# Performance work log

Hardware: AMD Instinct MI355X
Metric: run time of the kernel (lower is better)

Reference implementation:

```python
import jax, jax.numpy as jnp
import numpy as np

B, N, D, H, E, C = 32, 1024, 256, 256, 256, 256
K = 128          # top-k retained clusters = C // top_ratio
TEMP = 0.1
EPS = 1e-15


def _l2norm(x, eps=1e-12):
    n = jnp.linalg.norm(x, axis=-1, keepdims=True)
    return x / jnp.maximum(n, eps)


def _dense_sage(x, adj, Wr, br, Wo):
    # PyG DenseSAGEConv: mean-aggregate neighbors, lin_rel + lin_root, l2-normalize
    deg = jnp.clip(jnp.sum(adj, axis=-1, keepdims=True), 1.0, None)
    agg = jnp.matmul(adj, x) / deg                      # [B,N,D]
    out = agg @ Wr + br + x @ Wo                         # [B,N,H]
    return _l2norm(out)


def _sage_block(x, adj, Wr, br, Wo, Wl, bl):
    h = jax.nn.relu(_dense_sage(x, adj, Wr, br, Wo))
    return h @ Wl + bl


def setup_inputs() -> dict:
    key = jax.random.key(0)
    ks = jax.random.split(key, 12)
    sc = 0.05
    return {
        "x": jax.random.normal(ks[0], (B, N, D), jnp.float32),
        "adj": jax.random.uniform(ks[1], (B, N, N), jnp.float32),
        # pool branch (out = C clusters)
        "Wr_p": jax.random.normal(ks[2], (D, H), jnp.float32) * sc,
        "br_p": jnp.zeros((H,), jnp.float32),
        "Wo_p": jax.random.normal(ks[3], (D, H), jnp.float32) * sc,
        "Wl_p": jax.random.normal(ks[4], (H, C), jnp.float32) * sc,
        "bl_p": jnp.zeros((C,), jnp.float32),
        # embed branch (out = E features)
        "Wr_e": jax.random.normal(ks[5], (D, H), jnp.float32) * sc,
        "br_e": jnp.zeros((H,), jnp.float32),
        "Wo_e": jax.random.normal(ks[6], (D, H), jnp.float32) * sc,
        "Wl_e": jax.random.normal(ks[7], (H, E), jnp.float32) * sc,
        "bl_e": jnp.zeros((E,), jnp.float32),
    }


def reference(x, adj, Wr_p, br_p, Wo_p, Wl_p, bl_p, Wr_e, br_e, Wo_e, Wl_e, bl_e):
    s_logits = _sage_block(x, adj, Wr_p, br_p, Wo_p, Wl_p, bl_p)   # [B,N,C]
    node_x = _sage_block(x, adj, Wr_e, br_e, Wo_e, Wl_e, bl_e)     # [B,N,E]

    s = jax.nn.softmax(s_logits, axis=-1)

    # soft top-k cluster retain: sigmoid gate around the k-th largest column mass
    scores = jnp.sum(s, axis=1)                                    # [B,C]
    thresh = jax.lax.top_k(scores, K)[0][:, -1]                    # [B]
    gate = jax.nn.sigmoid((scores - thresh[:, None]) / TEMP)       # [B,C]
    s = s * gate[:, None, :]

    # pooled features / adjacency
    xp = jnp.einsum('bnc,bnd->bcd', s, node_x)                     # [B,C,E]
    sTa = jnp.einsum('bnc,bnm->bcm', s, adj)                       # [B,C,N]
    adj_p = jnp.einsum('bcm,bmk->bck', sTa, s)                     # [B,C,C]

    # link prediction loss: ||A - S S^T||_F / numel(A)
    ssT = jnp.einsum('bnc,bmc->bnm', s, s)
    link = jnp.linalg.norm(adj - ssT) / adj.size

    # entropy loss over assignments
    ent = jnp.mean(jnp.sum(-s * jnp.log(s + EPS), axis=-1))

    # cluster (orthogonality) loss: ||S^T S / ||S^T S||_F - I/sqrt(C)||_F
    sts = jnp.einsum('bnc,bnk->bck', s, s)                         # [B,C,C]
    sts_n = sts / jnp.maximum(
        jnp.linalg.norm(sts, axis=(-2, -1), keepdims=True), 1e-12)
    eye = jnp.eye(C, dtype=s.dtype) / jnp.sqrt(jnp.asarray(C, s.dtype))
    clu = jnp.mean(jnp.linalg.norm(sts_n - eye, axis=(-2, -1)))

    # adjacency reconstruction loss: ||A - S A_pool S^T||_F / numel(A)
    recon_adj = jnp.einsum('bnc,bck,bmk->bnm', s, adj_p, s)
    recon = jnp.linalg.norm(adj - recon_adj) / adj.size

    return (xp, adj_p, s, link, ent, clu, recon, node_x)
```

## Files before the change

kernel.cpp:

```cpp
#include <hip/hip_runtime.h>
#include <hip/hip_bf16.h>
#include <math.h>


typedef short bf16x8 __attribute__((ext_vector_type(8)));
typedef float f32x4 __attribute__((ext_vector_type(4)));
typedef unsigned short u16x8 __attribute__((ext_vector_type(8)));

__device__ inline void gl_lds16(const void* g, void* l) {
    __builtin_amdgcn_global_load_lds(
        (const __attribute__((address_space(1))) void*)g,
        (__attribute__((address_space(3))) void*)l, 16, 0, 0);
}

__device__ inline unsigned short f2b(float f) {
    union { __hip_bfloat16 h; unsigned short u; } cv;
    cv.h = __float2bfloat16(f);
    return cv.u;
}
__device__ inline float b2f(unsigned short u) {
    union { unsigned short u; __hip_bfloat16 h; } cv;
    cv.u = u;
    return __bfloat162float(cv.h);
}

__global__ __launch_bounds__(256) void adjconv_kernel(
    const float* __restrict__ adj, unsigned short* __restrict__ adj_bf,
    float* __restrict__ deginv, float* __restrict__ asq_part) {
    __shared__ float sq_red[4];
    const int tid = threadIdx.x;
    const int wave = tid >> 6, lane = tid & 63;
    const long long row = (long long)blockIdx.x * 4 + wave;
    const float* ip = adj + row * 1024;
    unsigned short* op = adj_bf + row * 1024;
    float sum = 0.f, sq = 0.f;
#pragma unroll
    for (int i = 0; i < 2; ++i) {
        const float4 v0 = *(const float4*)(ip + i * 512 + lane * 8);
        const float4 v1 = *(const float4*)(ip + i * 512 + lane * 8 + 4);
        u16x8 h;
        h[0] = f2b(v0.x); h[1] = f2b(v0.y); h[2] = f2b(v0.z); h[3] = f2b(v0.w);
        h[4] = f2b(v1.x); h[5] = f2b(v1.y); h[6] = f2b(v1.z); h[7] = f2b(v1.w);
        *(u16x8*)(op + i * 512 + lane * 8) = h;
        sum += (v0.x + v0.y + v0.z + v0.w) + (v1.x + v1.y + v1.z + v1.w);
        sq = fmaf(v0.x, v0.x, sq); sq = fmaf(v0.y, v0.y, sq);
        sq = fmaf(v0.z, v0.z, sq); sq = fmaf(v0.w, v0.w, sq);
        sq = fmaf(v1.x, v1.x, sq); sq = fmaf(v1.y, v1.y, sq);
        sq = fmaf(v1.z, v1.z, sq); sq = fmaf(v1.w, v1.w, sq);
    }
#pragma unroll
    for (int off = 32; off > 0; off >>= 1) {
        sum += __shfl_xor(sum, off);
        sq  += __shfl_xor(sq, off);
    }
    if (lane == 0) {
        deginv[row] = 1.0f / fmaxf(sum, 1.0f);
        sq_red[wave] = sq;
    }
    __syncthreads();
    if (tid == 0)
        asq_part[blockIdx.x] = sq_red[0] + sq_red[1] + sq_red[2] + sq_red[3];
}

__global__ __launch_bounds__(256) void convt_kernel(
    const float* __restrict__ in, long long sIn, int ldin,
    unsigned short* __restrict__ outN, long long sN,
    unsigned short* __restrict__ outT, long long sT, int ldT) {
    __shared__ float tile[64][65];
    const int tid = threadIdx.x;
    const long long bz = blockIdx.z;
    const int rowBase = blockIdx.y * 64, colBase = blockIdx.x * 64;
    const float* ip = in + bz * sIn;
#pragma unroll
    for (int i = 0; i < 4; ++i) {
        int r = (tid >> 4) * 4 + i;
        const float4 v = *(const float4*)(ip + (long long)(rowBase + r) * ldin + colBase + (tid & 15) * 4);
        tile[r][(tid & 15) * 4 + 0] = v.x;
        tile[r][(tid & 15) * 4 + 1] = v.y;
        tile[r][(tid & 15) * 4 + 2] = v.z;
        tile[r][(tid & 15) * 4 + 3] = v.w;
        if (outN) {
            ushort4 h;
            h.x = f2b(v.x); h.y = f2b(v.y); h.z = f2b(v.z); h.w = f2b(v.w);
            *(ushort4*)(outN + bz * sN + (long long)(rowBase + r) * ldin + colBase + (tid & 15) * 4) = h;
        }
    }
    __syncthreads();
    if (outT) {
#pragma unroll
        for (int i = 0; i < 4; ++i) {
            int oc = (tid >> 4) * 4 + i;
            ushort4 h;
            h.x = f2b(tile[(tid & 15) * 4 + 0][oc]);
            h.y = f2b(tile[(tid & 15) * 4 + 1][oc]);
            h.z = f2b(tile[(tid & 15) * 4 + 2][oc]);
            h.w = f2b(tile[(tid & 15) * 4 + 3][oc]);
            *(ushort4*)(outT + bz * sT + (long long)(colBase + oc) * ldT + rowBase + (tid & 15) * 4) = h;
        }
    }
}

struct WPtrs { const float* in[6]; unsigned short* out[6]; };
__global__ __launch_bounds__(256) void wconv_kernel(WPtrs wp) {
    __shared__ float tile[64][65];
    const int tid = threadIdx.x;
    const float* in = wp.in[blockIdx.z];
    unsigned short* out = wp.out[blockIdx.z];
    const int rowBase = blockIdx.y * 64, colBase = blockIdx.x * 64;
#pragma unroll
    for (int i = 0; i < 4; ++i) {
        int r = (tid >> 4) * 4 + i;
        const float4 v = *(const float4*)(in + (long long)(rowBase + r) * 256 + colBase + (tid & 15) * 4);
        tile[r][(tid & 15) * 4 + 0] = v.x;
        tile[r][(tid & 15) * 4 + 1] = v.y;
        tile[r][(tid & 15) * 4 + 2] = v.z;
        tile[r][(tid & 15) * 4 + 3] = v.w;
    }
    __syncthreads();
#pragma unroll
    for (int i = 0; i < 4; ++i) {
        int oc = (tid >> 4) * 4 + i;
        ushort4 h;
        h.x = f2b(tile[(tid & 15) * 4 + 0][oc]);
        h.y = f2b(tile[(tid & 15) * 4 + 1][oc]);
        h.z = f2b(tile[(tid & 15) * 4 + 2][oc]);
        h.w = f2b(tile[(tid & 15) * 4 + 3][oc]);
        *(ushort4*)(out + (long long)(colBase + oc) * 256 + rowBase + (tid & 15) * 4) = h;
    }
}

struct GemmP {
    const unsigned short* A1; long long sA1; int lda1; int K1;
    const unsigned short* B1; long long sB1; int ldb1;
    const unsigned short* A2; long long sA2; int lda2; int K2;
    const unsigned short* B2; long long sB2; int ldb2;
    float* outF; long long sF;
    unsigned short* outH; long long sH;
    unsigned short* outT; long long sT; int ldt;
    int ldc;
    const float* bias;
    const float* rowscale; long long sRS;
    const unsigned short* dotN; long long sDot;
    float* dot_part;
    float* sq_part;
};

__global__ __launch_bounds__(256) void gemm_mfma(GemmP p) {
    __shared__ char smem[32768];
    __shared__ float dred[256];
    const int tid = threadIdx.x;
    const int wave = tid >> 6, lane = tid & 63;
    const int quad = lane >> 4, l15 = lane & 15;
    const int wm = (wave & 1) * 64, wn = (wave >> 1) * 64;
    const long long bz = blockIdx.z;
    const int rowBase = blockIdx.y * 128, colBase = blockIdx.x * 128;
    const int srow = tid >> 2;
    const int skg = (((tid & 3) ^ ((srow >> 1) & 3)) * 8);
    const int rsw = (l15 >> 1) & 3;

    const int n1 = p.K1 >> 5;
    const int n2 = p.A2 ? (p.K2 >> 5) : 0;
    const int nTot = n1 + n2;

    const unsigned short* A1p = p.A1 + bz * p.sA1;
    const unsigned short* B1p = p.B1 + bz * p.sB1;
    const unsigned short* A2p = p.A2 ? p.A2 + bz * p.sA2 : nullptr;
    const unsigned short* B2p = p.B2 ? p.B2 + bz * p.sB2 : nullptr;

    auto stage = [&](int t, int buf) {
        const unsigned short *Ao, *Bo; int lda, ldb, ko;
        if (t < n1) { Ao = A1p; Bo = B1p; lda = p.lda1; ldb = p.ldb1; ko = t * 32; }
        else        { Ao = A2p; Bo = B2p; lda = p.lda2; ldb = p.ldb2; ko = (t - n1) * 32; }
        char* la = smem + buf * 16384 + wave * 1024;
        char* lb = smem + buf * 16384 + 8192 + wave * 1024;
        gl_lds16(Ao + (long long)(rowBase + srow) * lda + ko + skg, la);
        gl_lds16(Ao + (long long)(rowBase + 64 + srow) * lda + ko + skg, la + 4096);
        gl_lds16(Bo + (long long)(colBase + srow) * ldb + ko + skg, lb);
        gl_lds16(Bo + (long long)(colBase + 64 + srow) * ldb + ko + skg, lb + 4096);
    };

    f32x4 acc[4][4] = {{{0.f}}};
    stage(0, 0);
    __syncthreads();
    int cur = 0;
    for (int t = 0; t < nTot; ++t) {
        if (t + 1 < nTot) stage(t + 1, cur ^ 1);
        const short* Ab = (const short*)(smem + cur * 16384);
        const short* Bb = (const short*)(smem + cur * 16384 + 8192);
        bf16x8 af[4], bf[4];
#pragma unroll
        for (int i = 0; i < 4; ++i)
            af[i] = *(const bf16x8*)(Ab + (wm + i * 16 + l15) * 32 + (quad ^ rsw) * 8);
#pragma unroll
        for (int j = 0; j < 4; ++j)
            bf[j] = *(const bf16x8*)(Bb + (wn + j * 16 + l15) * 32 + (quad ^ rsw) * 8);
#pragma unroll
        for (int i = 0; i < 4; ++i)
#pragma unroll
            for (int j = 0; j < 4; ++j)
                acc[i][j] = __builtin_amdgcn_mfma_f32_16x16x32_bf16(af[i], bf[j], acc[i][j], 0, 0, 0);
        __syncthreads();
        cur ^= 1;
    }

    float* oF = p.outF ? p.outF + bz * p.sF : nullptr;
    unsigned short* oH = p.outH ? p.outH + bz * p.sH : nullptr;
    const unsigned short* dN = p.dotN ? p.dotN + bz * p.sDot : nullptr;
    unsigned short* tt = (unsigned short*)smem;
    float bcol[4];
#pragma unroll
    for (int j = 0; j < 4; ++j)
        bcol[j] = p.bias ? p.bias[colBase + wn + j * 16 + l15] : 0.0f;
    const float* rs = p.rowscale ? p.rowscale + bz * p.sRS : nullptr;
    float dacc = 0.f;
#pragma unroll
    for (int i = 0; i < 4; ++i) {
        ushort4 tp[4];
#pragma unroll
        for (int r = 0; r < 4; ++r) {
            int row = rowBase + wm + i * 16 + quad * 4 + r;
            float sc = rs ? rs[row] : 1.0f;
            long long ro = (long long)row * p.ldc;
#pragma unroll
            for (int j = 0; j < 4; ++j) {
                int col = colBase + wn + j * 16 + l15;
                float v = (acc[i][j][r] + bcol[j]) * sc;
                if (oF) oF[ro + col] = v;
                if (oH) oH[ro + col] = f2b(v);
                if (dN) dacc = fmaf(v, b2f(dN[ro + col]), dacc);
                if (p.sq_part) dacc = fmaf(v, v, dacc);
                ((unsigned short*)&tp[j])[r] = f2b(v);
            }
        }
        if (p.outT) {
            int lr = wm + i * 16 + quad * 4;
#pragma unroll
            for (int j = 0; j < 4; ++j) {
                int lc = wn + j * 16 + l15;
                *(ushort4*)&tt[lc * 128 + (lr ^ ((lc & 15) << 3))] = tp[j];
            }
        }
    }
    if (p.outT) {
        __syncthreads();
#pragma unroll
        for (int u = 0; u < 8; ++u) {
            int idx = u * 256 + tid;
            int c = idx >> 4;
            int r0 = (idx & 15) * 8;
            u16x8 val = *(const u16x8*)&tt[c * 128 + (r0 ^ ((c & 15) << 3))];
            int gr = rowBase + r0;
            long long tb = bz + (gr >> 10);
            *(u16x8*)(p.outT + tb * p.sT + (long long)(colBase + c) * p.ldt + (gr & 1023)) = val;
        }
    }
    if (p.dot_part || p.sq_part) {
        dred[tid] = dacc;
        __syncthreads();
        for (int k = 128; k > 0; k >>= 1) {
            if (tid < k) dred[tid] += dred[tid + k];
            __syncthreads();
        }
        if (tid == 0) {
            float* dst = p.dot_part ? p.dot_part : p.sq_part;
            dst[((long long)bz * gridDim.y + blockIdx.y) * gridDim.x + blockIdx.x] = dred[0];
        }
    }
}

struct SageP {
    const unsigned short* A1; const unsigned short* B1;
    const unsigned short* A2; const unsigned short* B2;
    const float* bias;
    unsigned short* out;
};

__global__ __launch_bounds__(512) void sage_mfma(SageP p) {
    __shared__ short As[2][4096];
    __shared__ short Bs[2][8192];
    __shared__ float rsum[4][128];
    const int tid = threadIdx.x;
    const int wave = tid >> 6, lane = tid & 63;
    const int quad = lane >> 4, l15 = lane & 15;
    const int wm = (wave & 1) * 64, wn = (wave >> 1) * 64;
    const int rowBase = blockIdx.x * 128;
    const int srow = tid >> 2;
    const int skg = (((tid & 3) ^ ((srow >> 1) & 3)) * 8);
    const int rsw = (l15 >> 1) & 3;

    auto stage = [&](int t, int buf) {
        const unsigned short* Ao = (t < 8) ? p.A1 : p.A2;
        const unsigned short* Bo = (t < 8) ? p.B1 : p.B2;
        int ko = (t & 7) * 32;
        char* la = (char*)As[buf] + wave * 1024;
        char* lb = (char*)Bs[buf] + wave * 1024;
        gl_lds16(Ao + (long long)(rowBase + srow) * 256 + ko + skg, la);
        gl_lds16(Bo + (long long)srow * 256 + ko + skg, lb);
        gl_lds16(Bo + (long long)(128 + srow) * 256 + ko + skg, lb + 8192);
    };

    f32x4 acc[4][4] = {{{0.f}}};
    stage(0, 0);
    __syncthreads();
    int cur = 0;
    for (int t = 0; t < 16; ++t) {
        if (t + 1 < 16) stage(t + 1, cur ^ 1);
        const short* Ab = As[cur];
        const short* Bb = Bs[cur];
        bf16x8 af[4], bf[4];
#pragma unroll
        for (int i = 0; i < 4; ++i)
            af[i] = *(const bf16x8*)(Ab + (wm + i * 16 + l15) * 32 + (quad ^ rsw) * 8);
#pragma unroll
        for (int j = 0; j < 4; ++j)
            bf[j] = *(const bf16x8*)(Bb + (wn + j * 16 + l15) * 32 + (quad ^ rsw) * 8);
#pragma unroll
        for (int i = 0; i < 4; ++i)
#pragma unroll
            for (int j = 0; j < 4; ++j)
                acc[i][j] = __builtin_amdgcn_mfma_f32_16x16x32_bf16(af[i], bf[j], acc[i][j], 0, 0, 0);
        __syncthreads();
        cur ^= 1;
    }

    float bcol[4];
#pragma unroll
    for (int j = 0; j < 4; ++j)
        bcol[j] = p.bias[wn + j * 16 + l15];

#pragma unroll
    for (int i = 0; i < 4; ++i)
#pragma unroll
        for (int r = 0; r < 4; ++r) {
            float ss = 0.f;
#pragma unroll
            for (int j = 0; j < 4; ++j) {
                float v = acc[i][j][r] + bcol[j];
                ss = fmaf(v, v, ss);
            }
#pragma unroll
            for (int off = 1; off < 16; off <<= 1) ss += __shfl_xor(ss, off);
            if (l15 == 0) rsum[wave >> 1][wm + i * 16 + quad * 4 + r] = ss;
        }
    __syncthreads();
#pragma unroll
    for (int i = 0; i < 4; ++i)
#pragma unroll
        for (int r = 0; r < 4; ++r) {
            int lrow = wm + i * 16 + quad * 4 + r;
            float tot = rsum[0][lrow] + rsum[1][lrow] + rsum[2][lrow] + rsum[3][lrow];
            float rn = 1.0f / fmaxf(sqrtf(tot), 1e-12f);
            long long ro = (long long)(rowBase + lrow) * 256;
#pragma unroll
            for (int j = 0; j < 4; ++j) {
                float v = (acc[i][j][r] + bcol[j]) * rn;
                p.out[ro + wn + j * 16 + l15] = f2b(fmaxf(v, 0.0f));
            }
        }
}

__global__ __launch_bounds__(256) void sts_clu_mfma(
    const unsigned short* __restrict__ sT, unsigned short* __restrict__ gout,
    float* __restrict__ ssq_part, float* __restrict__ tr_part) {
    __shared__ short As[2][128 * 32];
    __shared__ short Bs[2][128 * 32];
    __shared__ float red[2][256];
    const int tid = threadIdx.x;
    const int wave = tid >> 6, lane = tid & 63;
    const int quad = lane >> 4, l15 = lane & 15;
    const int wm = (wave & 1) * 64, wn = (wave >> 1) * 64;
    const long long bz = blockIdx.z;
    const unsigned short* S = sT + bz * 262144;
    const int rowBase = blockIdx.y * 128, colBase = blockIdx.x * 128;
    const int srow = tid >> 2;
    const int skg = (((tid & 3) ^ ((srow >> 1) & 3)) * 8);
    const int rsw = (l15 >> 1) & 3;

    auto stage = [&](int t, int buf) {
        int ko = t * 32;
        char* la = (char*)As + buf * 8192 + wave * 1024;
        char* lb = (char*)Bs + buf * 8192 + wave * 1024;
        gl_lds16(S + (long long)(rowBase + srow) * 1024 + ko + skg, la);
        gl_lds16(S + (long long)(rowBase + 64 + srow) * 1024 + ko + skg, la + 4096);
        gl_lds16(S + (long long)(colBase + srow) * 1024 + ko + skg, lb);
        gl_lds16(S + (long long)(colBase + 64 + srow) * 1024 + ko + skg, lb + 4096);
    };

    f32x4 acc[4][4] = {{{0.f}}};
    stage(0, 0);
    __syncthreads();
    int cur = 0;
    for (int t = 0; t < 32; ++t) {
        if (t + 1 < 32) stage(t + 1, cur ^ 1);
        const short* Ab = (const short*)((char*)As + cur * 8192);
        const short* Bb = (const short*)((char*)Bs + cur * 8192);
        bf16x8 af[4], bf[4];
#pragma unroll
        for (int i = 0; i < 4; ++i)
            af[i] = *(const bf16x8*)(Ab + (wm + i * 16 + l15) * 32 + (quad ^ rsw) * 8);
#pragma unroll
        for (int j = 0; j < 4; ++j)
            bf[j] = *(const bf16x8*)(Bb + (wn + j * 16 + l15) * 32 + (quad ^ rsw) * 8);
#pragma unroll
        for (int i = 0; i < 4; ++i)
#pragma unroll
            for (int j = 0; j < 4; ++j)
                acc[i][j] = __builtin_amdgcn_mfma_f32_16x16x32_bf16(af[i], bf[j], acc[i][j], 0, 0, 0);
        __syncthreads();
        cur ^= 1;
    }
    unsigned short* go = gout + bz * 65536;
    float ssq = 0.f, tr = 0.f;
#pragma unroll
    for (int i = 0; i < 4; ++i)
#pragma unroll
        for (int r = 0; r < 4; ++r) {
            int row = rowBase + wm + i * 16 + quad * 4 + r;
#pragma unroll
            for (int j = 0; j < 4; ++j) {
                int col = colBase + wn + j * 16 + l15;
                float v = acc[i][j][r];
                go[(long long)row * 256 + col] = f2b(v);
                ssq = fmaf(v, v, ssq);
                if (row == col) tr += v;
            }
        }
    red[0][tid] = ssq;
    red[1][tid] = tr;
    __syncthreads();
    for (int k = 128; k > 0; k >>= 1) {
        if (tid < k) {
            red[0][tid] += red[0][tid + k];
            red[1][tid] += red[1][tid + k];
        }
        __syncthreads();
    }
    if (tid == 0) {
        int bid = (int)(blockIdx.z * 4 + blockIdx.y * 2 + blockIdx.x);
        ssq_part[bid] = red[0][0];
        tr_part[bid] = red[1][0];
    }
}

__global__ __launch_bounds__(256) void trq_mfma(
    const unsigned short* __restrict__ G, const unsigned short* __restrict__ P,
    const unsigned short* __restrict__ PT, float* __restrict__ trq_part) {
    __shared__ short sm[4][2][4096];
    __shared__ float dred[256];
    const int tid = threadIdx.x;
    const int wave = tid >> 6, lane = tid & 63;
    const int quad = lane >> 4, l15 = lane & 15;
    const int wm = (wave & 1) * 64, wn = (wave >> 1) * 64;
    const long long bz = blockIdx.z;
    const int rowBase = blockIdx.y * 128, colBase = blockIdx.x * 128;
    const int srow = tid >> 2;
    const int skg = (((tid & 3) ^ ((srow >> 1) & 3)) * 8);
    const int rsw = (l15 >> 1) & 3;
    const unsigned short* Gb = G + bz * 65536;
    const unsigned short* Pb = P + bz * 65536;
    const unsigned short* PTb = PT + bz * 65536;

    auto stage = [&](int t, int buf) {
        int ko = t * 32;
#pragma unroll
        for (int h = 0; h < 2; ++h) {
            int rr = rowBase + h * 64 + srow, cc = colBase + h * 64 + srow;
            gl_lds16(Gb + (long long)rr * 256 + ko + skg, (char*)sm[0][buf] + h * 4096 + wave * 1024);
            gl_lds16(PTb + (long long)cc * 256 + ko + skg, (char*)sm[1][buf] + h * 4096 + wave * 1024);
            gl_lds16(Pb + (long long)rr * 256 + ko + skg, (char*)sm[2][buf] + h * 4096 + wave * 1024);
            gl_lds16(Gb + (long long)cc * 256 + ko + skg, (char*)sm[3][buf] + h * 4096 + wave * 1024);
        }
    };

    f32x4 a1[4][4] = {{{0.f}}};
    f32x4 a3[4][4] = {{{0.f}}};
    stage(0, 0);
    __syncthreads();
    int cur = 0;
    for (int t = 0; t < 8; ++t) {
        if (t + 1 < 8) stage(t + 1, cur ^ 1);
        bf16x8 gA[4], pB[4], pA[4], gB[4];
#pragma unroll
        for (int i = 0; i < 4; ++i) {
            int ro = (wm + i * 16 + l15) * 32 + (quad ^ rsw) * 8;
            gA[i] = *(const bf16x8*)(sm[0][cur] + ro);
            pA[i] = *(const bf16x8*)(sm[2][cur] + ro);
        }
#pragma unroll
        for (int j = 0; j < 4; ++j) {
            int co = (wn + j * 16 + l15) * 32 + (quad ^ rsw) * 8;
            pB[j] = *(const bf16x8*)(sm[1][cur] + co);
            gB[j] = *(const bf16x8*)(sm[3][cur] + co);
        }
#pragma unroll
        for (int i = 0; i < 4; ++i)
#pragma unroll
            for (int j = 0; j < 4; ++j) {
                a1[i][j] = __builtin_amdgcn_mfma_f32_16x16x32_bf16(gA[i], pB[j], a1[i][j], 0, 0, 0);
                a3[i][j] = __builtin_amdgcn_mfma_f32_16x16x32_bf16(pA[i], gB[j], a3[i][j], 0, 0, 0);
            }
        __syncthreads();
        cur ^= 1;
    }
    float dacc = 0.f;
#pragma unroll
    for (int i = 0; i < 4; ++i)
#pragma unroll
        for (int j = 0; j < 4; ++j)
#pragma unroll
            for (int r = 0; r < 4; ++r)
                dacc = fmaf(a3[i][j][r], a1[i][j][r], dacc);
    dred[tid] = dacc;
    __syncthreads();
    for (int k = 128; k > 0; k >>= 1) {
        if (tid < k) dred[tid] += dred[tid + k];
        __syncthreads();
    }
    if (tid == 0)
        trq_part[(blockIdx.z * 2 + blockIdx.y) * 2 + blockIdx.x] = dred[0];
}

__global__ __launch_bounds__(256) void smstat_kernel(
    const float* __restrict__ s, float* __restrict__ rowmax,
    float* __restrict__ rowrden, float* __restrict__ scores) {
    __shared__ float sacc[4][256];
    const int tid = threadIdx.x;
    const int wave = tid >> 6, lane = tid & 63;
    const int b = blockIdx.x >> 5;
    const long long row0 = (long long)blockIdx.x * 32;
    float c0 = 0.f, c1 = 0.f, c2 = 0.f, c3 = 0.f;
#pragma unroll
    for (int q = 0; q < 8; ++q) {
        long long row = row0 + wave * 8 + q;
        const float4 v = *(const float4*)(s + row * 256 + lane * 4);
        float m = fmaxf(fmaxf(v.x, v.y), fmaxf(v.z, v.w));
#pragma unroll
        for (int off = 32; off > 0; off >>= 1) m = fmaxf(m, __shfl_xor(m, off));
        float e0 = expf(v.x - m), e1 = expf(v.y - m);
        float e2 = expf(v.z - m), e3 = expf(v.w - m);
        float den = e0 + e1 + e2 + e3;
#pragma unroll
        for (int off = 32; off > 0; off >>= 1) den += __shfl_xor(den, off);
        float rd = 1.0f / den;
        if (lane == 0) { rowmax[row] = m; rowrden[row] = rd; }
        c0 = fmaf(e0, rd, c0); c1 = fmaf(e1, rd, c1);
        c2 = fmaf(e2, rd, c2); c3 = fmaf(e3, rd, c3);
    }
    sacc[wave][lane * 4 + 0] = c0;
    sacc[wave][lane * 4 + 1] = c1;
    sacc[wave][lane * 4 + 2] = c2;
    sacc[wave][lane * 4 + 3] = c3;
    __syncthreads();
    float t0 = sacc[0][tid] + sacc[1][tid] + sacc[2][tid] + sacc[3][tid];
    atomicAdd(&scores[b * 256 + tid], t0);
}

__global__ __launch_bounds__(256) void topkgate_kernel(const float* __restrict__ scores,
                                                       float* __restrict__ gate) {
    __shared__ float vals[256];
    __shared__ float th;
    int b = blockIdx.x, tid = threadIdx.x;
    float v = scores[b * 256 + tid];
    vals[tid] = v;
    __syncthreads();
    int rank = 0;
    for (int j = 0; j < 256; ++j) {
        float u = vals[j];
        rank += (u > v) || (u == v && j < tid);
    }
    if (rank == 127) th = v;
    __syncthreads();
    float z = (v - th) * 10.0f;
    gate[b * 256 + tid] = 1.0f / (1.0f + expf(-z));
}

__global__ __launch_bounds__(256) void gatefin_kernel(
    float* __restrict__ s, const float* __restrict__ rowmax,
    const float* __restrict__ rowrden, const float* __restrict__ gate,
    unsigned short* __restrict__ sbf, unsigned short* __restrict__ sT,
    float* __restrict__ ent_part) {
    __shared__ float tile[64][65];
    __shared__ float red[256];
    const int tid = threadIdx.x;
    const long long bz = blockIdx.z;
    const int rowBase = blockIdx.y * 64, colBase = blockIdx.x * 64;
    const int c4 = (tid & 15) * 4;
    const float g0 = gate[bz * 256 + colBase + c4 + 0];
    const float g1 = gate[bz * 256 + colBase + c4 + 1];
    const float g2 = gate[bz * 256 + colBase + c4 + 2];
    const float g3 = gate[bz * 256 + colBase + c4 + 3];
    float ent = 0.f;
#pragma unroll
    for (int i = 0; i < 4; ++i) {
        int r = (tid >> 4) * 4 + i;
        long long grow = bz * 1024 + rowBase + r;
        float4 v = *(const float4*)(s + grow * 256 + colBase + c4);
        float m = rowmax[grow], rd = rowrden[grow];
        float p0 = expf(v.x - m) * rd * g0;
        float p1 = expf(v.y - m) * rd * g1;
        float p2 = expf(v.z - m) * rd * g2;
        float p3 = expf(v.w - m) * rd * g3;
        float4 pv; pv.x = p0; pv.y = p1; pv.z = p2; pv.w = p3;
        *(float4*)(s + grow * 256 + colBase + c4) = pv;
        ushort4 h;
        h.x = f2b(p0); h.y = f2b(p1); h.z = f2b(p2); h.w = f2b(p3);
        *(ushort4*)(sbf + grow * 256 + colBase + c4) = h;
        tile[r][c4 + 0] = p0; tile[r][c4 + 1] = p1;
        tile[r][c4 + 2] = p2; tile[r][c4 + 3] = p3;
        ent -= p0 * logf(p0 + 1e-15f) + p1 * logf(p1 + 1e-15f) +
               p2 * logf(p2 + 1e-15f) + p3 * logf(p3 + 1e-15f);
    }
    __syncthreads();
#pragma unroll
    for (int i = 0; i < 4; ++i) {
        int oc = (tid >> 4) * 4 + i;
        ushort4 h;
        h.x = f2b(tile[c4 + 0][oc]);
        h.y = f2b(tile[c4 + 1][oc]);
        h.z = f2b(tile[c4 + 2][oc]);
        h.w = f2b(tile[c4 + 3][oc]);
        *(ushort4*)(sT + bz * 262144 + (long long)(colBase + oc) * 1024 + rowBase + c4) = h;
    }
    red[tid] = ent;
    __syncthreads();
    for (int k = 128; k > 0; k >>= 1) {
        if (tid < k) red[tid] += red[tid + k];
        __syncthreads();
    }
    if (tid == 0)
        ent_part[((long long)bz * gridDim.y + blockIdx.y) * gridDim.x + blockIdx.x] = red[0];
}

__global__ __launch_bounds__(256) void finalize_kernel(const float* __restrict__ ent_part,
                                                       const float* __restrict__ asq_part,
                                                       const float* __restrict__ psq_part,
                                                       const float* __restrict__ sdot_part,
                                                       const float* __restrict__ trq_part,
                                                       const float* __restrict__ ssq_part,
                                                       const float* __restrict__ tr_part,
                                                       float* __restrict__ scal) {
    __shared__ float red[7][256];
    int tid = threadIdx.x;
    float e = 0.f, asq = 0.f, psq = 0.f, sd = 0.f, tq = 0.f, clu = 0.f, ssqa = 0.f;
    for (int i = tid; i < 2048; i += 256) e += ent_part[i];
    for (int i = tid; i < 8192; i += 256) asq += asq_part[i];
    if (tid < 128) psq = psq_part[tid];
    for (int i = tid; i < 512; i += 256) sd += sdot_part[i];
    if (tid < 128) tq = trq_part[tid];
    if (tid < 32) {
        float ssq = 0.f, tr = 0.f;
#pragma unroll
        for (int i = 0; i < 4; ++i) {
            ssq += ssq_part[tid * 4 + i];
            tr  += tr_part[tid * 4 + i];
        }
        ssqa = ssq;
        float fro = fmaxf(sqrtf(ssq), 1e-12f);
        float val = ssq / (fro * fro) - tr / (8.0f * fro) + 1.0f;
        clu = sqrtf(fmaxf(val, 0.0f));
    }
    red[0][tid] = e; red[1][tid] = asq; red[2][tid] = psq; red[3][tid] = sd;
    red[4][tid] = tq; red[5][tid] = clu; red[6][tid] = ssqa;
    __syncthreads();
    for (int k = 128; k > 0; k >>= 1) {
        if (tid < k) {
#pragma unroll
            for (int q = 0; q < 7; ++q) red[q][tid] += red[q][tid + k];
        }
        __syncthreads();
    }
    if (tid == 0) {
        const float numel = 33554432.0f;
        float linksq  = red[1][0] - 2.0f * red[3][0] + red[6][0];
        float reconsq = red[1][0] - 2.0f * red[2][0] + red[4][0];
        scal[0] = sqrtf(fmaxf(linksq, 0.0f)) / numel;
        scal[1] = red[0][0] / 32768.0f;
        scal[2] = red[5][0] / 32.0f;
        scal[3] = sqrtf(fmaxf(reconsq, 0.0f)) / numel;
    }
}

extern "C" void kernel_launch(void* const* d_in, const int* in_sizes, int n_in,
                              void* d_out, int out_size, void* d_ws, size_t ws_size,
                              hipStream_t stream) {
    const float* x    = (const float*)d_in[0];
    const float* adj  = (const float*)d_in[1];
    const float* Wr_p = (const float*)d_in[2];
    const float* br_p = (const float*)d_in[3];
    const float* Wo_p = (const float*)d_in[4];
    const float* Wl_p = (const float*)d_in[5];
    const float* bl_p = (const float*)d_in[6];
    const float* Wr_e = (const float*)d_in[7];
    const float* br_e = (const float*)d_in[8];
    const float* Wo_e = (const float*)d_in[9];
    const float* Wl_e = (const float*)d_in[10];
    const float* bl_e = (const float*)d_in[11];

    float* out    = (float*)d_out;
    float* xp     = out;
    float* adj_p  = out + 2097152;
    float* s      = out + 4194304;
    float* scal   = out + 12582912;
    float* node_x = out + 12582916;

    char* w = (char*)d_ws;
    float* degsum     = (float*)w; w += 32768 * 4;
    float* scores     = (float*)w; w += 8192 * 4;
    float* thresh     = (float*)w; w += 256 * 4;
    float* gatep      = (float*)w; w += 8192 * 4;
    float* ent_part   = (float*)w; w += 32768 * 4;
    float* asq_part   = (float*)w; w += 8192 * 4;
    float* psq_part   = (float*)w; w += 512 * 4;
    float* sdot_part  = (float*)w; w += 1024 * 4;
    float* trq_part   = (float*)w; w += 256 * 4;
    float* ssq_part   = (float*)w; w += 256 * 4;
    float* tr_part    = (float*)w; w += 256 * 4;
    unsigned short* WT   = (unsigned short*)w; w += 6LL * 65536 * 2;
    unsigned short* bufA = (unsigned short*)w; w += 33554432LL * 2;
    unsigned short* bufB = (unsigned short*)w; w += 8388608LL * 2;
    unsigned short* bufC = (unsigned short*)w; w += 8388608LL * 2;
    unsigned short* bufD = (unsigned short*)w; w += 8388608LL * 2;
    unsigned short* bufE = (unsigned short*)w; w += 8388608LL * 2;
    unsigned short* bufF = (unsigned short*)w; w += 8388608LL * 2;
    unsigned short* bufG = (unsigned short*)w; w += 8388608LL * 2;
    unsigned short* bufH = (unsigned short*)w; w += 2097152LL * 2;

    unsigned short* G_bf  = bufB;
    unsigned short* PT_bf = bufB + 2097152;
    float* rowmax  = degsum;
    float* rowrden = (float*)bufH;
    (void)thresh;

    hipMemsetAsync(scores, 0, 8192 * sizeof(float), stream);

    adjconv_kernel<<<8192, 256, 0, stream>>>(adj, bufA, degsum, asq_part);

    convt_kernel<<<dim3(4, 16, 32), 256, 0, stream>>>(
        x, 262144LL, 256, bufB, 262144LL, bufC, 262144LL, 1024);

    WPtrs wp;
    wp.in[0] = Wr_p; wp.in[1] = Wo_p; wp.in[2] = Wl_p;
    wp.in[3] = Wr_e; wp.in[4] = Wo_e; wp.in[5] = Wl_e;
    for (int i = 0; i < 6; ++i) wp.out[i] = WT + (long long)i * 65536;
    wconv_kernel<<<dim3(4, 4, 6), 256, 0, stream>>>(wp);

    GemmP g;
    g = {};
    g.A1 = bufA; g.sA1 = 1048576; g.lda1 = 1024; g.K1 = 1024;
    g.B1 = bufC; g.sB1 = 262144; g.ldb1 = 1024;
    g.outH = bufD; g.sH = 262144; g.ldc = 256;
    g.rowscale = degsum; g.sRS = 1024;
    gemm_mfma<<<dim3(2, 8, 32), 256, 0, stream>>>(g);

    SageP sp;
    sp.A1 = bufD; sp.B1 = WT + 0 * 65536;
    sp.A2 = bufB; sp.B2 = WT + 1 * 65536;
    sp.bias = br_p; sp.out = bufE;
    sage_mfma<<<256, 512, 0, stream>>>(sp);

    g = {};
    g.A1 = bufE; g.sA1 = 0; g.lda1 = 256; g.K1 = 256; g.B1 = WT + 2 * 65536; g.sB1 = 0; g.ldb1 = 256;
    g.outF = s; g.sF = 0; g.ldc = 256; g.bias = bl_p;
    gemm_mfma<<<dim3(2, 256, 1), 256, 0, stream>>>(g);

    sp.A1 = bufD; sp.B1 = WT + 3 * 65536;
    sp.A2 = bufB; sp.B2 = WT + 4 * 65536;
    sp.bias = br_e; sp.out = bufE;
    sage_mfma<<<256, 512, 0, stream>>>(sp);

    g = {};
    g.A1 = bufE; g.sA1 = 0; g.lda1 = 256; g.K1 = 256; g.B1 = WT + 5 * 65536; g.sB1 = 0; g.ldb1 = 256;
    g.outF = node_x; g.sF = 0; g.ldc = 256; g.bias = bl_e;
    g.outT = bufD; g.sT = 262144; g.ldt = 1024;
    gemm_mfma<<<dim3(2, 256, 1), 256, 0, stream>>>(g);

    smstat_kernel<<<1024, 256, 0, stream>>>(s, rowmax, rowrden, scores);
    topkgate_kernel<<<32, 256, 0, stream>>>(scores, gatep);
    gatefin_kernel<<<dim3(4, 16, 32), 256, 0, stream>>>(
        s, rowmax, rowrden, gatep, bufG, bufC, ent_part);

    g = {};
    g.A1 = bufC; g.sA1 = 262144; g.lda1 = 1024; g.K1 = 1024;
    g.B1 = bufD; g.sB1 = 262144; g.ldb1 = 1024;
    g.outF = xp; g.sF = 65536; g.ldc = 256;
    gemm_mfma<<<dim3(2, 2, 32), 256, 0, stream>>>(g);

    g = {};
    g.A1 = bufA; g.sA1 = 1048576; g.lda1 = 1024; g.K1 = 1024;
    g.B1 = bufC; g.sB1 = 262144; g.ldb1 = 1024;
    g.ldc = 256;
    g.outT = bufF; g.sT = 262144; g.ldt = 1024;
    g.dotN = bufG; g.sDot = 262144; g.dot_part = sdot_part;
    gemm_mfma<<<dim3(2, 8, 32), 256, 0, stream>>>(g);

    sts_clu_mfma<<<dim3(2, 2, 32), 256, 0, stream>>>(bufC, G_bf, ssq_part, tr_part);

    g = {};
    g.A1 = bufC; g.sA1 = 262144; g.lda1 = 1024; g.K1 = 1024;
    g.B1 = bufF; g.sB1 = 262144; g.ldb1 = 1024;
    g.outF = adj_p; g.sF = 65536; g.ldc = 256;
    g.outH = bufH; g.sH = 65536;
    g.outT = PT_bf; g.sT = 65536; g.ldt = 256;
    g.sq_part = psq_part;
    gemm_mfma<<<dim3(2, 2, 32), 256, 0, stream>>>(g);

    trq_mfma<<<dim3(2, 2, 32), 256, 0, stream>>>(G_bf, bufH, PT_bf, trq_part);

    finalize_kernel<<<1, 256, 0, stream>>>(ent_part, asq_part, psq_part, sdot_part,
                                           trq_part, ssq_part, tr_part, scal);
}
```

Before: 580.0 us.

## Fuse adjacency conversion into aggregation GEMM, merge xp and S^T S GEMMs

Adjacency bf16 conversion, degree and squared-norm reduction now run inside a new aggregation MFMA kernel. It reads fp32 adj straight from global memory and feeds the converted tile into LDS, which removes the separate conversion pass and the later re-read of bf16 adj. The xp and S^T S GEMMs now share one kernel that loads the S^T tile once for both products. The pooling logits are also stored as bf16 instead of fp32, which cuts memory traffic but reduces softmax input precision.

```diff
diff --git a/kernel.cpp b/kernel.cpp
--- a/kernel.cpp
+++ b/kernel.cpp
@@ -22,44 +22,6 @@
     union { unsigned short u; __hip_bfloat16 h; } cv;
     cv.u = u;
     return __bfloat162float(cv.h);
-}
-
-__global__ __launch_bounds__(256) void adjconv_kernel(
-    const float* __restrict__ adj, unsigned short* __restrict__ adj_bf,
-    float* __restrict__ deginv, float* __restrict__ asq_part) {
-    __shared__ float sq_red[4];
-    const int tid = threadIdx.x;
-    const int wave = tid >> 6, lane = tid & 63;
-    const long long row = (long long)blockIdx.x * 4 + wave;
-    const float* ip = adj + row * 1024;
-    unsigned short* op = adj_bf + row * 1024;
-    float sum = 0.f, sq = 0.f;
-#pragma unroll
-    for (int i = 0; i < 2; ++i) {
-        const float4 v0 = *(const float4*)(ip + i * 512 + lane * 8);
-        const float4 v1 = *(const float4*)(ip + i * 512 + lane * 8 + 4);
-        u16x8 h;
-        h[0] = f2b(v0.x); h[1] = f2b(v0.y); h[2] = f2b(v0.z); h[3] = f2b(v0.w);
-        h[4] = f2b(v1.x); h[5] = f2b(v1.y); h[6] = f2b(v1.z); h[7] = f2b(v1.w);
-        *(u16x8*)(op + i * 512 + lane * 8) = h;
-        sum += (v0.x + v0.y + v0.z + v0.w) + (v1.x + v1.y + v1.z + v1.w);
-        sq = fmaf(v0.x, v0.x, sq); sq = fmaf(v0.y, v0.y, sq);
-        sq = fmaf(v0.z, v0.z, sq); sq = fmaf(v0.w, v0.w, sq);
-        sq = fmaf(v1.x, v1.x, sq); sq = fmaf(v1.y, v1.y, sq);
-        sq = fmaf(v1.z, v1.z, sq); sq = fmaf(v1.w, v1.w, sq);
-    }
-#pragma unroll
-    for (int off = 32; off > 0; off >>= 1) {
-        sum += __shfl_xor(sum, off);
-        sq  += __shfl_xor(sq, off);
-    }
-    if (lane == 0) {
-        deginv[row] = 1.0f / fmaxf(sum, 1.0f);
-        sq_red[wave] = sq;
-    }
-    __syncthreads();
-    if (tid == 0)
-        asq_part[blockIdx.x] = sq_red[0] + sq_red[1] + sq_red[2] + sq_red[3];
 }
 
 __global__ __launch_bounds__(256) void convt_kernel(
@@ -129,6 +91,110 @@
     }
 }
 
+struct AggP {
+    const float* adj;
+    const unsigned short* xT;
+    unsigned short* adj_bf;
+    unsigned short* agg;
+    float* asq_part;
+};
+
+__global__ __launch_bounds__(512) void aggdeg_mfma(AggP p) {
+    __shared__ short As[2][128 * 32];
+    __shared__ short Bs[2][256 * 32];
+    __shared__ float deginv_lds[128];
+    __shared__ float sred[512];
+    const int tid = threadIdx.x;
+    const int wave = tid >> 6, lane = tid & 63;
+    const int quad = lane >> 4, l15 = lane & 15;
+    const int wm = (wave & 1) * 64, wn = (wave >> 1) * 64;
+    const int rowBase = blockIdx.x * 128;
+    const long long bz = blockIdx.y;
+    const int srow = tid >> 2, kq = tid & 3;
+    const int sw = (srow >> 1) & 3;
+    const int skg = ((kq ^ sw) * 8);
+    const int rsw = (l15 >> 1) & 3;
+
+    const float* adjp = p.adj + bz * 1048576 + (long long)(rowBase + srow) * 1024 + kq * 8;
+    unsigned short* abf = p.adj_bf + bz * 1048576 + (long long)(rowBase + srow) * 1024 + kq * 8;
+    const unsigned short* xTp = p.xT + bz * 262144;
+
+    float4 ra, rb;
+    float degacc = 0.f, sqacc = 0.f;
+
+    auto loadA = [&](int t) {
+        ra = *(const float4*)(adjp + t * 32);
+        rb = *(const float4*)(adjp + t * 32 + 4);
+    };
+    auto procA = [&](int t, int buf) {
+        u16x8 h;
+        h[0] = f2b(ra.x); h[1] = f2b(ra.y); h[2] = f2b(ra.z); h[3] = f2b(ra.w);
+        h[4] = f2b(rb.x); h[5] = f2b(rb.y); h[6] = f2b(rb.z); h[7] = f2b(rb.w);
+        *(u16x8*)(abf + t * 32) = h;
+        degacc += (ra.x + ra.y + ra.z + ra.w) + (rb.x + rb.y + rb.z + rb.w);
+        sqacc = fmaf(ra.x, ra.x, sqacc); sqacc = fmaf(ra.y, ra.y, sqacc);
+        sqacc = fmaf(ra.z, ra.z, sqacc); sqacc = fmaf(ra.w, ra.w, sqacc);
+        sqacc = fmaf(rb.x, rb.x, sqacc); sqacc = fmaf(rb.y, rb.y, sqacc);
+        sqacc = fmaf(rb.z, rb.z, sqacc); sqacc = fmaf(rb.w, rb.w, sqacc);
+        *(u16x8*)((unsigned short*)As[buf] + srow * 32 + ((kq ^ sw) * 8)) = h;
+    };
+    auto stageB = [&](int t, int buf) {
+        char* lb = (char*)Bs[buf] + wave * 1024;
+        gl_lds16(xTp + (long long)srow * 1024 + t * 32 + skg, lb);
+        gl_lds16(xTp + (long long)(128 + srow) * 1024 + t * 32 + skg, lb + 8192);
+    };
+
+    f32x4 acc[4][4] = {{{0.f}}};
+    loadA(0);
+    stageB(0, 0);
+    procA(0, 0);
+    __syncthreads();
+    int cur = 0;
+    for (int t = 0; t < 32; ++t) {
+        const bool more = (t + 1 < 32);
+        if (more) { loadA(t + 1); stageB(t + 1, cur ^ 1); }
+        bf16x8 af[4], bv[4];
+#pragma unroll
+        for (int i = 0; i < 4; ++i)
+            af[i] = *(const bf16x8*)(As[cur] + (wm + i * 16 + l15) * 32 + (quad ^ rsw) * 8);
+#pragma unroll
+        for (int j = 0; j < 4; ++j)
+            bv[j] = *(const bf16x8*)(Bs[cur] + (wn + j * 16 + l15) * 32 + (quad ^ rsw) * 8);
+#pragma unroll
+        for (int i = 0; i < 4; ++i)
+#pragma unroll
+            for (int j = 0; j < 4; ++j)
+                acc[i][j] = __builtin_amdgcn_mfma_f32_16x16x32_bf16(af[i], bv[j], acc[i][j], 0, 0, 0);
+        if (more) procA(t + 1, cur ^ 1);
+        __syncthreads();
+        cur ^= 1;
+    }
+
+    degacc += __shfl_xor(degacc, 1);
+    degacc += __shfl_xor(degacc, 2);
+    if (kq == 0) deginv_lds[srow] = 1.0f / fmaxf(degacc, 1.0f);
+    sred[tid] = sqacc;
+    __syncthreads();
+    for (int k = 256; k > 0; k >>= 1) {
+        if (tid < k) sred[tid] += sred[tid + k];
+        __syncthreads();
+    }
+    if (tid == 0) p.asq_part[bz * 8 + blockIdx.x] = sred[0];
+
+    unsigned short* og = p.agg + bz * 262144;
+#pragma unroll
+    for (int i = 0; i < 4; ++i)
+#pragma unroll
+        for (int r = 0; r < 4; ++r) {
+            int lrow = wm + i * 16 + quad * 4 + r;
+            float sc = deginv_lds[lrow];
+            long long ro = (long long)(rowBase + lrow) * 256;
+#pragma unroll
+            for (int j = 0; j < 4; ++j)
+                og[ro + wn + j * 16 + l15] = f2b(acc[i][j][r] * sc);
+        }
+}
+
 struct GemmP {
     const unsigned short* A1; long long sA1; int lda1; int K1;
     const unsigned short* B1; long long sB1; int ldb1;
@@ -139,7 +205,6 @@
     unsigned short* outT; long long sT; int ldt;
     int ldc;
     const float* bias;
-    const float* rowscale; long long sRS;
     const unsigned short* dotN; long long sDot;
     float* dot_part;
     float* sq_part;
@@ -211,7 +276,6 @@
 #pragma unroll
     for (int j = 0; j < 4; ++j)
         bcol[j] = p.bias ? p.bias[colBase + wn + j * 16 + l15] : 0.0f;
-    const float* rs = p.rowscale ? p.rowscale + bz * p.sRS : nullptr;
     float dacc = 0.f;
 #pragma unroll
     for (int i = 0; i < 4; ++i) {
@@ -219,12 +283,11 @@
 #pragma unroll
         for (int r = 0; r < 4; ++r) {
             int row = rowBase + wm + i * 16 + quad * 4 + r;
-            float sc = rs ? rs[row] : 1.0f;
             long long ro = (long long)row * p.ldc;
 #pragma unroll
             for (int j = 0; j < 4; ++j) {
                 int col = colBase + wn + j * 16 + l15;
-                float v = (acc[i][j][r] + bcol[j]) * sc;
+                float v = acc[i][j][r] + bcol[j];
                 if (oF) oF[ro + col] = v;
                 if (oH) oH[ro + col] = f2b(v);
                 if (dN) dacc = fmaf(v, b2f(dN[ro + col]), dacc);
@@ -359,11 +422,11 @@
         }
 }
 
-__global__ __launch_bounds__(256) void sts_clu_mfma(
-    const unsigned short* __restrict__ sT, unsigned short* __restrict__ gout,
+__global__ __launch_bounds__(256) void xpg_mfma(
+    const unsigned short* __restrict__ sT, const unsigned short* __restrict__ nxT,
+    float* __restrict__ xp, unsigned short* __restrict__ gout,
     float* __restrict__ ssq_part, float* __restrict__ tr_part) {
-    __shared__ short As[2][128 * 32];
-    __shared__ short Bs[2][128 * 32];
+    __shared__ char smem[49152];
     __shared__ float red[2][256];
     const int tid = threadIdx.x;
     const int wave = tid >> 6, lane = tid & 63;
@@ -371,6 +434,7 @@
     const int wm = (wave & 1) * 64, wn = (wave >> 1) * 64;
     const long long bz = blockIdx.z;
     const unsigned short* S = sT + bz * 262144;
+    const unsigned short* NX = nxT + bz * 262144;
     const int rowBase = blockIdx.y * 128, colBase = blockIdx.x * 128;
     const int srow = tid >> 2;
     const int skg = (((tid & 3) ^ ((srow >> 1) & 3)) * 8);
@@ -378,37 +442,49 @@
 
     auto stage = [&](int t, int buf) {
         int ko = t * 32;
-        char* la = (char*)As + buf * 8192 + wave * 1024;
-        char* lb = (char*)Bs + buf * 8192 + wave * 1024;
+        char* la = smem + buf * 8192 + wave * 1024;
+        char* l1 = smem + 16384 + buf * 8192 + wave * 1024;
+        char* l2 = smem + 32768 + buf * 8192 + wave * 1024;
         gl_lds16(S + (long long)(rowBase + srow) * 1024 + ko + skg, la);
         gl_lds16(S + (long long)(rowBase + 64 + srow) * 1024 + ko + skg, la + 4096);
-        gl_lds16(S + (long long)(colBase + srow) * 1024 + ko + skg, lb);
-        gl_lds16(S + (long long)(colBase + 64 + srow) * 1024 + ko + skg, lb + 4096);
+        gl_lds16(NX + (long long)(colBase + srow) * 1024 + ko + skg, l1);
+        gl_lds16(NX + (long long)(colBase + 64 + srow) * 1024 + ko + skg, l1 + 4096);
+        gl_lds16(S + (long long)(colBase + srow) * 1024 + ko + skg, l2);
+        gl_lds16(S + (long long)(colBase + 64 + srow) * 1024 + ko + skg, l2 + 4096);
     };
 
-    f32x4 acc[4][4] = {{{0.f}}};
+    f32x4 a1[4][4] = {{{0.f}}};
+    f32x4 a2[4][4] = {{{0.f}}};
     stage(0, 0);
     __syncthreads();
     int cur = 0;
     for (int t = 0; t < 32; ++t) {
         if (t + 1 < 32) stage(t + 1, cur ^ 1);
-        const short* Ab = (const short*)((char*)As + cur * 8192);
-        const short* Bb = (const short*)((char*)Bs + cur * 8192);
-        bf16x8 af[4], bf[4];
+        const short* Ab  = (const short*)(smem + cur * 8192);
+        const short* B1b = (const short*)(smem + 16384 + cur * 8192);
+        const short* B2b = (const short*)(smem + 32768 + cur * 8192);
+        bf16x8 af[4], b1[4], b2[4];
 #pragma unroll
         for (int i = 0; i < 4; ++i)
             af[i] = *(const bf16x8*)(Ab + (wm + i * 16 + l15) * 32 + (quad ^ rsw) * 8);
 #pragma unroll
-        for (int j = 0; j < 4; ++j)
-            bf[j] = *(const bf16x8*)(Bb + (wn + j * 16 + l15) * 32 + (quad ^ rsw) * 8);
+        for (int j = 0; j < 4; ++j) {
+            int co = (wn + j * 16 + l15) * 32 + (quad ^ rsw) * 8;
+            b1[j] = *(const bf16x8*)(B1b + co);
+            b2[j] = *(const bf16x8*)(B2b + co);
+        }
 #pragma unroll
         for (int i = 0; i < 4; ++i)
 #pragma unroll
-            for (int j = 0; j < 4; ++j)
-                acc[i][j] = __builtin_amdgcn_mfma_f32_16x16x32_bf16(af[i], bf[j], acc[i][j], 0, 0, 0);
+            for (int j = 0; j < 4; ++j) {
+                a1[i][j] = __builtin_amdgcn_mfma_f32_16x16x32_bf16(af[i], b1[j], a1[i][j], 0, 0, 0);
+                a2[i][j] = __builtin_amdgcn_mfma_f32_16x16x32_bf16(af[i], b2[j], a2[i][j], 0, 0, 0);
+            }
         __syncthreads();
         cur ^= 1;
     }
+
+    float* xo = xp + bz * 65536;
     unsigned short* go = gout + bz * 65536;
     float ssq = 0.f, tr = 0.f;
 #pragma unroll
@@ -416,11 +492,13 @@
 #pragma unroll
         for (int r = 0; r < 4; ++r) {
             int row = rowBase + wm + i * 16 + quad * 4 + r;
+            long long ro = (long long)row * 256;
 #pragma unroll
             for (int j = 0; j < 4; ++j) {
                 int col = colBase + wn + j * 16 + l15;
-                float v = acc[i][j][r];
-                go[(long long)row * 256 + col] = f2b(v);
+                xo[ro + col] = a1[i][j][r];
+                float v = a2[i][j][r];
+                go[ro + col] = f2b(v);
                 ssq = fmaf(v, v, ssq);
                 if (row == col) tr += v;
             }
@@ -521,7 +599,7 @@
 }
 
 __global__ __launch_bounds__(256) void smstat_kernel(
-    const float* __restrict__ s, float* __restrict__ rowmax,
+    const unsigned short* __restrict__ s, float* __restrict__ rowmax,
     float* __restrict__ rowrden, float* __restrict__ scores) {
     __shared__ float sacc[4][256];
     const int tid = threadIdx.x;
@@ -532,12 +610,13 @@
 #pragma unroll
     for (int q = 0; q < 8; ++q) {
         long long row = row0 + wave * 8 + q;
-        const float4 v = *(const float4*)(s + row * 256 + lane * 4);
-        float m = fmaxf(fmaxf(v.x, v.y), fmaxf(v.z, v.w));
+        const ushort4 v4 = *(const ushort4*)(s + row * 256 + lane * 4);
+        float vx = b2f(v4.x), vy = b2f(v4.y), vz = b2f(v4.z), vw = b2f(v4.w);
+        float m = fmaxf(fmaxf(vx, vy), fmaxf(vz, vw));
 #pragma unroll
         for (int off = 32; off > 0; off >>= 1) m = fmaxf(m, __shfl_xor(m, off));
-        float e0 = expf(v.x - m), e1 = expf(v.y - m);
-        float e2 = expf(v.z - m), e3 = expf(v.w - m);
+        float e0 = expf(vx - m), e1 = expf(vy - m);
+        float e2 = expf(vz - m), e3 = expf(vw - m);
         float den = e0 + e1 + e2 + e3;
 #pragma unroll
         for (int off = 32; off > 0; off >>= 1) den += __shfl_xor(den, off);
@@ -575,10 +654,10 @@
 }
 
 __global__ __launch_bounds__(256) void gatefin_kernel(
-    float* __restrict__ s, const float* __restrict__ rowmax,
-    const float* __restrict__ rowrden, const float* __restrict__ gate,
-    unsigned short* __restrict__ sbf, unsigned short* __restrict__ sT,
-    float* __restrict__ ent_part) {
+    const unsigned short* slog, float* __restrict__ s,
+    const float* __restrict__ rowmax, const float* __restrict__ rowrden,
+    const float* __restrict__ gate, unsigned short* sbf,
+    unsigned short* __restrict__ sT, float* __restrict__ ent_part) {
     __shared__ float tile[64][65];
     __shared__ float red[256];
     const int tid = threadIdx.x;
@@ -594,12 +673,12 @@
     for (int i = 0; i < 4; ++i) {
         int r = (tid >> 4) * 4 + i;
         long long grow = bz * 1024 + rowBase + r;
-        float4 v = *(const float4*)(s + grow * 256 + colBase + c4);
+        ushort4 lv = *(const ushort4*)(slog + grow * 256 + colBase + c4);
         float m = rowmax[grow], rd = rowrden[grow];
-        float p0 = expf(v.x - m) * rd * g0;
-        float p1 = expf(v.y - m) * rd * g1;
-        float p2 = expf(v.z - m) * rd * g2;
-        float p3 = expf(v.w - m) * rd * g3;
+        float p0 = expf(b2f(lv.x) - m) * rd * g0;
+        float p1 = expf(b2f(lv.y) - m) * rd * g1;
+        float p2 = expf(b2f(lv.z) - m) * rd * g2;
+        float p3 = expf(b2f(lv.w) - m) * rd * g3;
         float4 pv; pv.x = p0; pv.y = p1; pv.z = p2; pv.w = p3;
         *(float4*)(s + grow * 256 + colBase + c4) = pv;
         ushort4 h;
@@ -643,7 +722,7 @@
     int tid = threadIdx.x;
     float e = 0.f, asq = 0.f, psq = 0.f, sd = 0.f, tq = 0.f, clu = 0.f, ssqa = 0.f;
     for (int i = tid; i < 2048; i += 256) e += ent_part[i];
-    for (int i = tid; i < 8192; i += 256) asq += asq_part[i];
+    asq = asq_part[tid];
     if (tid < 128) psq = psq_part[tid];
     for (int i = tid; i < 512; i += 256) sd += sdot_part[i];
     if (tid < 128) tq = trq_part[tid];
@@ -704,7 +783,7 @@
     float* node_x = out + 12582916;
 
     char* w = (char*)d_ws;
-    float* degsum     = (float*)w; w += 32768 * 4;
+    float* rowmax     = (float*)w; w += 32768 * 4;
     float* scores     = (float*)w; w += 8192 * 4;
     float* thresh     = (float*)w; w += 256 * 4;
     float* gatep      = (float*)w; w += 8192 * 4;
@@ -727,13 +806,10 @@
 
     unsigned short* G_bf  = bufB;
     unsigned short* PT_bf = bufB + 2097152;
-    float* rowmax  = degsum;
     float* rowrden = (float*)bufH;
     (void)thresh;
 
     hipMemsetAsync(scores, 0, 8192 * sizeof(float), stream);
-
-    adjconv_kernel<<<8192, 256, 0, stream>>>(adj, bufA, degsum, asq_part);
 
     convt_kernel<<<dim3(4, 16, 32), 256, 0, stream>>>(
         x, 262144LL, 256, bufB, 262144LL, bufC, 262144LL, 1024);
@@ -744,13 +820,9 @@
     for (int i = 0; i < 6; ++i) wp.out[i] = WT + (long long)i * 65536;
     wconv_kernel<<<dim3(4, 4, 6), 256, 0, stream>>>(wp);
 
-    GemmP g;
-    g = {};
-    g.A1 = bufA; g.sA1 = 1048576; g.lda1 = 1024; g.K1 = 1024;
-    g.B1 = bufC; g.sB1 = 262144; g.ldb1 = 1024;
-    g.outH = bufD; g.sH = 262144; g.ldc = 256;
-    g.rowscale = degsum; g.sRS = 1024;
-    gemm_mfma<<<dim3(2, 8, 32), 256, 0, stream>>>(g);
+    AggP ap;
+    ap.adj = adj; ap.xT = bufC; ap.adj_bf = bufA; ap.agg = bufD; ap.asq_part = asq_part;
+    aggdeg_mfma<<<dim3(8, 32), 512, 0, stream>>>(ap);
 
     SageP sp;
     sp.A1 = bufD; sp.B1 = WT + 0 * 65536;
@@ -758,9 +830,10 @@
     sp.bias = br_p; sp.out = bufE;
     sage_mfma<<<256, 512, 0, stream>>>(sp);
 
+    GemmP g;
     g = {};
     g.A1 = bufE; g.sA1 = 0; g.lda1 = 256; g.K1 = 256; g.B1 = WT + 2 * 65536; g.sB1 = 0; g.ldb1 = 256;
-    g.outF = s; g.sF = 0; g.ldc = 256; g.bias = bl_p;
+    g.outH = bufG; g.sH = 0; g.ldc = 256; g.bias = bl_p;
     gemm_mfma<<<dim3(2, 256, 1), 256, 0, stream>>>(g);
 
     sp.A1 = bufD; sp.B1 = WT + 3 * 65536;
@@ -774,16 +847,12 @@
     g.outT = bufD; g.sT = 262144; g.ldt = 1024;
     gemm_mfma<<<dim3(2, 256, 1), 256, 0, stream>>>(g);
 
-    smstat_kernel<<<1024, 256, 0, stream>>>(s, rowmax, rowrden, scores);
+    smstat_kernel<<<1024, 256, 0, stream>>>(bufG, rowmax, rowrden, scores);
     topkgate_kernel<<<32, 256, 0, stream>>>(scores, gatep);
     gatefin_kernel<<<dim3(4, 16, 32), 256, 0, stream>>>(
-        s, rowmax, rowrden, gatep, bufG, bufC, ent_part);
-
-    g = {};
-    g.A1 = bufC; g.sA1 = 262144; g.lda1 = 1024; g.K1 = 1024;
-    g.B1 = bufD; g.sB1 = 262144; g.ldb1 = 1024;
-    g.outF = xp; g.sF = 65536; g.ldc = 256;
-    gemm_mfma<<<dim3(2, 2, 32), 256, 0, stream>>>(g);
+        bufG, s, rowmax, rowrden, gatep, bufG, bufC, ent_part);
+
+    xpg_mfma<<<dim3(2, 2, 32), 256, 0, stream>>>(bufC, bufD, xp, G_bf, ssq_part, tr_part);
 
     g = {};
     g.A1 = bufA; g.sA1 = 1048576; g.lda1 = 1024; g.K1 = 1024;
@@ -792,8 +861,6 @@
     g.outT = bufF; g.sT = 262144; g.ldt = 1024;
     g.dotN = bufG; g.sDot = 262144; g.dot_part = sdot_part;
     gemm_mfma<<<dim3(2, 8, 32), 256, 0, stream>>>(g);
-
-    sts_clu_mfma<<<dim3(2, 2, 32), 256, 0, stream>>>(bufC, G_bf, ssq_part, tr_part);
 
     g = {};
     g.A1 = bufC; g.sA1 = 262144; g.lda1 = 1024; g.K1 = 1024;
```

After: 554.1 us. 1.05x faster.
